# Optimization experiments

Hardware: AMD Instinct MI355X
Metric: run time of the kernel (lower is better)

## Reference

```python
import jax, jax.numpy as jnp
import numpy as np

HIDDEN_DIM = 2048
NUM_EXPERTS = 64
TOP_K = 8
NUM_TOKENS = 16384


def setup_inputs() -> dict:
    key = jax.random.key(0)
    k_x, k_w, k_b = jax.random.split(key, 3)
    X = jax.random.normal(k_x, (NUM_TOKENS, HIDDEN_DIM), dtype=jnp.float32)
    # nn.Linear(hidden_dim, num_experts): weight [out, in], bias [out]
    bound = 1.0 / np.sqrt(HIDDEN_DIM)
    W_gate = jax.random.uniform(k_w, (NUM_EXPERTS, HIDDEN_DIM), jnp.float32, -bound, bound)
    b_gate = jax.random.uniform(k_b, (NUM_EXPERTS,), jnp.float32, -bound, bound)
    return {"X": X, "W_gate": W_gate, "b_gate": b_gate}


def reference(X, W_gate, b_gate):
    # gate linear: [T, H] @ [H, E] + [E] -> [T, E]
    router_logits = jnp.einsum('th,eh->te', X, W_gate) + b_gate
    # softmax in float32 (matches dtype=torch.float)
    router_probs = jax.nn.softmax(router_logits.astype(jnp.float32), axis=-1)
    # top-k over experts: [T, K]
    router_weights, selected_experts_indices = jax.lax.top_k(router_probs, TOP_K)
    router_weights = router_weights / jnp.sum(router_weights, axis=-1, keepdims=True)
    router_weights = router_weights.astype(X.dtype)
    # one-hot [T, K, E] -> permute(2,1,0) -> [E, K, T]
    expert_mask = jax.nn.one_hot(selected_experts_indices, NUM_EXPERTS, dtype=jnp.int64 if jax.config.jax_enable_x64 else jnp.int32)
    expert_mask = jnp.transpose(expert_mask, (2, 1, 0))
    return (router_logits, router_weights, selected_experts_indices.astype(jnp.int32), expert_mask)
```

## Files before the change

### kernel.cpp

```cpp
#include <hip/hip_runtime.h>

#define NT 16384
#define NH 2048
#define NE 64
#define TOPK 8

#define TB 32
#define KSTEPS 64
#define KQ 4
#define KSW (KSTEPS / KQ)

#define LOFF 0
#define WOFF (NT * NE)
#define IOFF (WOFF + NT * TOPK)
#define MOFF (IOFF + NT * TOPK)

typedef __attribute__((ext_vector_type(8))) short short8;
typedef __attribute__((ext_vector_type(4))) float floatx4;

union FragU { uint4 u; short8 s; };

__device__ __forceinline__ unsigned pack3(float a, float b, unsigned& w1, unsigned& w2) {
    unsigned au = __float_as_uint(a), bu = __float_as_uint(b);
    unsigned ah0 = au & 0xFFFF0000u, bh0 = bu & 0xFFFF0000u;
    float ra = a - __uint_as_float(ah0);
    float rb = b - __uint_as_float(bh0);
    unsigned ar = __float_as_uint(ra), br = __float_as_uint(rb);
    unsigned ah1 = ar & 0xFFFF0000u, bh1 = br & 0xFFFF0000u;
    float sa = ra - __uint_as_float(ah1);
    float sb = rb - __uint_as_float(bh1);
    w1 = bh1 | (ah1 >> 16);
    w2 = (__float_as_uint(sb) & 0xFFFF0000u) | (__float_as_uint(sa) >> 16);
    return bh0 | (ah0 >> 16);
}

__global__ __launch_bounds__(64)
void wconv_kernel(const float* __restrict__ Wg, uint4* __restrict__ wsp) {
    const int b = blockIdx.x;
    const int t = b >> 2, g = b & 3;
    const int l = threadIdx.x;
    const int e  = g * 16 + (l & 15);
    const int k0 = t * 32 + (l >> 4) * 8;
    const float* src = Wg + (size_t)e * NH + k0;
    float4 w0 = *(const float4*)src;
    float4 w1 = *(const float4*)(src + 4);
    unsigned u1[4], u2[4];
    uint4 p0;
    p0.x = pack3(w0.x, w0.y, u1[0], u2[0]);
    p0.y = pack3(w0.z, w0.w, u1[1], u2[1]);
    p0.z = pack3(w1.x, w1.y, u1[2], u2[2]);
    p0.w = pack3(w1.z, w1.w, u1[3], u2[3]);
    uint4* dst = wsp + (size_t)((t * 4 + g) * 3) * 64 + l;
    dst[0]   = p0;
    dst[64]  = make_uint4(u1[0], u1[1], u1[2], u1[3]);
    dst[128] = make_uint4(u2[0], u2[1], u2[2], u2[3]);
}

__global__ __launch_bounds__(256, 2)
void router_kernel(const float* __restrict__ X, const uint4* __restrict__ wsp,
                   const float* __restrict__ bg, float* __restrict__ out) {
    __shared__ __align__(16) float P[KQ][TB][68];
    __shared__ __align__(16) float Ls[TB][68];

    const int tid = threadIdx.x;
    const int kh  = tid >> 6;
    const int l   = tid & 63;
    const int lr  = l & 15, lq = l >> 4;
    const int tbase = blockIdx.x * TB;

    floatx4 acc[2][4];
#pragma unroll
    for (int a = 0; a < 2; a++)
#pragma unroll
        for (int g = 0; g < 4; g++) acc[a][g] = (floatx4)0.0f;

    const float* xp0 = X + (size_t)(tbase + lr) * NH + kh * (KSW * 32) + lq * 8;
    const float* xp1 = xp0 + (size_t)16 * NH;
    const uint4* wp = wsp + (size_t)(kh * KSW) * 12 * 64 + l;

    float4 a0lo = *(const float4*)xp0;
    float4 a0hi = *(const float4*)(xp0 + 4);
    float4 a1lo = *(const float4*)xp1;
    float4 a1hi = *(const float4*)(xp1 + 4);

    {
        float4 z = make_float4(0.f, 0.f, 0.f, 0.f);
#pragma unroll
        for (int m = 0; m < 16; m++) {
            int f2  = tid + 256 * m;
            int seg = f2 >> 3;
            int off = (f2 & 7) << 2;
            *(float4*)(out + MOFF + (size_t)seg * NT + tbase + off) = z;
        }
    }

#pragma unroll 2
    for (int t = 0; t < KSW; t++) {
        FragU b[4][3];
        const uint4* wt = wp + t * 768;
#pragma unroll
        for (int g = 0; g < 4; g++)
#pragma unroll
            for (int p = 0; p < 3; p++)
                b[g][p].u = wt[(g * 3 + p) * 64];

        FragU af[2][3];
        {
            unsigned u1[4], u2[4];
            uint4 q;
            q.x = pack3(a0lo.x, a0lo.y, u1[0], u2[0]);
            q.y = pack3(a0lo.z, a0lo.w, u1[1], u2[1]);
            q.z = pack3(a0hi.x, a0hi.y, u1[2], u2[2]);
            q.w = pack3(a0hi.z, a0hi.w, u1[3], u2[3]);
            af[0][0].u = q;
            af[0][1].u = make_uint4(u1[0], u1[1], u1[2], u1[3]);
            af[0][2].u = make_uint4(u2[0], u2[1], u2[2], u2[3]);
            q.x = pack3(a1lo.x, a1lo.y, u1[0], u2[0]);
            q.y = pack3(a1lo.z, a1lo.w, u1[1], u2[1]);
            q.z = pack3(a1hi.x, a1hi.y, u1[2], u2[2]);
            q.w = pack3(a1hi.z, a1hi.w, u1[3], u2[3]);
            af[1][0].u = q;
            af[1][1].u = make_uint4(u1[0], u1[1], u1[2], u1[3]);
            af[1][2].u = make_uint4(u2[0], u2[1], u2[2], u2[3]);
        }

        if (t + 1 < KSW) {
            const float* nx0 = xp0 + (t + 1) * 32;
            const float* nx1 = xp1 + (t + 1) * 32;
            a0lo = *(const float4*)nx0;
            a0hi = *(const float4*)(nx0 + 4);
            a1lo = *(const float4*)nx1;
            a1hi = *(const float4*)(nx1 + 4);
        }

#pragma unroll
        for (int g = 0; g < 4; g++)
#pragma unroll
            for (int a = 0; a < 2; a++) {
                acc[a][g] = __builtin_amdgcn_mfma_f32_16x16x32_bf16(af[a][0].s, b[g][0].s, acc[a][g], 0, 0, 0);
                acc[a][g] = __builtin_amdgcn_mfma_f32_16x16x32_bf16(af[a][0].s, b[g][1].s, acc[a][g], 0, 0, 0);
                acc[a][g] = __builtin_amdgcn_mfma_f32_16x16x32_bf16(af[a][1].s, b[g][0].s, acc[a][g], 0, 0, 0);
                acc[a][g] = __builtin_amdgcn_mfma_f32_16x16x32_bf16(af[a][1].s, b[g][1].s, acc[a][g], 0, 0, 0);
                acc[a][g] = __builtin_amdgcn_mfma_f32_16x16x32_bf16(af[a][0].s, b[g][2].s, acc[a][g], 0, 0, 0);
                acc[a][g] = __builtin_amdgcn_mfma_f32_16x16x32_bf16(af[a][2].s, b[g][0].s, acc[a][g], 0, 0, 0);
            }
    }

#pragma unroll
    for (int a = 0; a < 2; a++)
#pragma unroll
        for (int g = 0; g < 4; g++)
#pragma unroll
            for (int r = 0; r < 4; r++)
                P[kh][a * 16 + lq * 4 + r][g * 16 + lr] = acc[a][g][r];
    __syncthreads();

#pragma unroll
    for (int jj = 0; jj < 2; jj++) {
        int f4  = tid + 256 * jj;
        int tok = f4 >> 4;
        int e4  = (f4 & 15) << 2;
        float4 s0 = *(float4*)&P[0][tok][e4];
        float4 s1 = *(float4*)&P[1][tok][e4];
        float4 s2 = *(float4*)&P[2][tok][e4];
        float4 s3 = *(float4*)&P[3][tok][e4];
        float4 bb = *(const float4*)(bg + e4);
        float4 v;
        v.x = s0.x + s1.x + s2.x + s3.x + bb.x;
        v.y = s0.y + s1.y + s2.y + s3.y + bb.y;
        v.z = s0.z + s1.z + s2.z + s3.z + bb.z;
        v.w = s0.w + s1.w + s2.w + s3.w + bb.w;
        *(float4*)&Ls[tok][e4] = v;
        *(float4*)(out + LOFF + (size_t)tbase * NE + (size_t)f4 * 4) = v;
    }
    __syncthreads();

    const int tok = (tid >> 6) * 8 + ((tid & 63) >> 3);
    const int el  = tid & 7;
    float4 va = *(float4*)&Ls[tok][el * 8];
    float4 vb = *(float4*)&Ls[tok][el * 8 + 4];
    float v[8] = {va.x, va.y, va.z, va.w, vb.x, vb.y, vb.z, vb.w};

    unsigned msk = 0;
    float m0 = 0.f, ssum = 0.f, myv = 0.f;
    int myi = 0;
#pragma unroll
    for (int r = 0; r < 8; r++) {
        float bv = -3.0e38f; int bi = 64;
#pragma unroll
        for (int j = 0; j < 8; j++) {
            bool better = (((msk >> j) & 1u) == 0u) && (v[j] > bv);
            bv = better ? v[j] : bv;
            bi = better ? (el * 8 + j) : bi;
        }
#pragma unroll
        for (int s2 = 1; s2 < 8; s2 <<= 1) {
            float ov = __shfl_xor(bv, s2);
            int   oi = __shfl_xor(bi, s2);
            bool take = (ov > bv) || (ov == bv && oi < bi);
            bv = take ? ov : bv;
            bi = take ? oi : bi;
        }
        if ((bi >> 3) == el) msk |= (1u << (bi & 7));
        if (r == 0) m0 = bv;
        ssum += __expf(bv - m0);
        if (r == el) { myv = bv; myi = bi; }
    }
    float w = __expf(myv - m0) / ssum;
    size_t gt = (size_t)(tbase + tok);
    out[WOFF + gt * TOPK + el] = w;
    out[IOFF + gt * TOPK + el] = (float)myi;
    out[MOFF + (size_t)myi * (TOPK * NT) + (size_t)el * NT + gt] = 1.0f;
}

extern "C" void kernel_launch(void* const* d_in, const int* in_sizes, int n_in,
                              void* d_out, int out_size, void* d_ws, size_t ws_size,
                              hipStream_t stream) {
    const float* X  = (const float*)d_in[0];
    const float* Wg = (const float*)d_in[1];
    const float* bg = (const float*)d_in[2];
    float* out = (float*)d_out;
    uint4* wsp = (uint4*)d_ws;

    hipLaunchKernelGGL(wconv_kernel, dim3(KSTEPS * 4), dim3(64), 0, stream, Wg, wsp);
    hipLaunchKernelGGL(router_kernel, dim3(NT / TB), dim3(256), 0, stream,
                       X, (const uint4*)wsp, bg, out);
}
```

Baseline: 223.2 us.

## Split token halves across doubled wave count and raise MFMA priority

The router kernel now launches 512 threads per block. Each wave handles one 16-token half and one K quarter, where before each wave computed both halves. This halves per-wave accumulator and fragment registers, so occupancy can rise under launch_bounds(512,4). The MFMA block is also wrapped in s_setprio to favor matrix issue. The trade-off is that each wave now loads the W fragments for its own token half, doubling W fragment traffic per block.

After: 241.4 us. 1.08x slower.

```diff
diff --git a/kernel.cpp b/kernel.cpp
--- a/kernel.cpp
+++ b/kernel.cpp
@@ -56,38 +56,35 @@
     dst[128] = make_uint4(u2[0], u2[1], u2[2], u2[3]);
 }
 
-__global__ __launch_bounds__(256, 2)
+__global__ __launch_bounds__(512, 4)
 void router_kernel(const float* __restrict__ X, const uint4* __restrict__ wsp,
                    const float* __restrict__ bg, float* __restrict__ out) {
     __shared__ __align__(16) float P[KQ][TB][68];
     __shared__ __align__(16) float Ls[TB][68];
 
     const int tid = threadIdx.x;
-    const int kh  = tid >> 6;
+    const int w   = tid >> 6;
+    const int kh  = w & 3;
+    const int th  = w >> 2;
     const int l   = tid & 63;
     const int lr  = l & 15, lq = l >> 4;
     const int tbase = blockIdx.x * TB;
 
-    floatx4 acc[2][4];
-#pragma unroll
-    for (int a = 0; a < 2; a++)
-#pragma unroll
-        for (int g = 0; g < 4; g++) acc[a][g] = (floatx4)0.0f;
-
-    const float* xp0 = X + (size_t)(tbase + lr) * NH + kh * (KSW * 32) + lq * 8;
-    const float* xp1 = xp0 + (size_t)16 * NH;
+    floatx4 acc[4];
+#pragma unroll
+    for (int g = 0; g < 4; g++) acc[g] = (floatx4)0.0f;
+
+    const float* xp0 = X + (size_t)(tbase + th * 16 + lr) * NH + kh * (KSW * 32) + lq * 8;
     const uint4* wp = wsp + (size_t)(kh * KSW) * 12 * 64 + l;
 
     float4 a0lo = *(const float4*)xp0;
     float4 a0hi = *(const float4*)(xp0 + 4);
-    float4 a1lo = *(const float4*)xp1;
-    float4 a1hi = *(const float4*)(xp1 + 4);
 
     {
         float4 z = make_float4(0.f, 0.f, 0.f, 0.f);
 #pragma unroll
-        for (int m = 0; m < 16; m++) {
-            int f2  = tid + 256 * m;
+        for (int m = 0; m < 8; m++) {
+            int f2  = tid + 512 * m;
             int seg = f2 >> 3;
             int off = (f2 & 7) << 2;
             *(float4*)(out + MOFF + (size_t)seg * NT + tbase + off) = z;
@@ -104,7 +101,7 @@
             for (int p = 0; p < 3; p++)
                 b[g][p].u = wt[(g * 3 + p) * 64];
 
-        FragU af[2][3];
+        FragU af[3];
         {
             unsigned u1[4], u2[4];
             uint4 q;
@@ -112,52 +109,39 @@
             q.y = pack3(a0lo.z, a0lo.w, u1[1], u2[1]);
             q.z = pack3(a0hi.x, a0hi.y, u1[2], u2[2]);
             q.w = pack3(a0hi.z, a0hi.w, u1[3], u2[3]);
-            af[0][0].u = q;
-            af[0][1].u = make_uint4(u1[0], u1[1], u1[2], u1[3]);
-            af[0][2].u = make_uint4(u2[0], u2[1], u2[2], u2[3]);
-            q.x = pack3(a1lo.x, a1lo.y, u1[0], u2[0]);
-            q.y = pack3(a1lo.z, a1lo.w, u1[1], u2[1]);
-            q.z = pack3(a1hi.x, a1hi.y, u1[2], u2[2]);
-            q.w = pack3(a1hi.z, a1hi.w, u1[3], u2[3]);
-            af[1][0].u = q;
-            af[1][1].u = make_uint4(u1[0], u1[1], u1[2], u1[3]);
-            af[1][2].u = make_uint4(u2[0], u2[1], u2[2], u2[3]);
+            af[0].u = q;
+            af[1].u = make_uint4(u1[0], u1[1], u1[2], u1[3]);
+            af[2].u = make_uint4(u2[0], u2[1], u2[2], u2[3]);
         }
 
         if (t + 1 < KSW) {
             const float* nx0 = xp0 + (t + 1) * 32;
-            const float* nx1 = xp1 + (t + 1) * 32;
             a0lo = *(const float4*)nx0;
             a0hi = *(const float4*)(nx0 + 4);
-            a1lo = *(const float4*)nx1;
-            a1hi = *(const float4*)(nx1 + 4);
-        }
-
-#pragma unroll
-        for (int g = 0; g < 4; g++)
-#pragma unroll
-            for (int a = 0; a < 2; a++) {
-                acc[a][g] = __builtin_amdgcn_mfma_f32_16x16x32_bf16(af[a][0].s, b[g][0].s, acc[a][g], 0, 0, 0);
-                acc[a][g] = __builtin_amdgcn_mfma_f32_16x16x32_bf16(af[a][0].s, b[g][1].s, acc[a][g], 0, 0, 0);
-                acc[a][g] = __builtin_amdgcn_mfma_f32_16x16x32_bf16(af[a][1].s, b[g][0].s, acc[a][g], 0, 0, 0);
-                acc[a][g] = __builtin_amdgcn_mfma_f32_16x16x32_bf16(af[a][1].s, b[g][1].s, acc[a][g], 0, 0, 0);
-                acc[a][g] = __builtin_amdgcn_mfma_f32_16x16x32_bf16(af[a][0].s, b[g][2].s, acc[a][g], 0, 0, 0);
-                acc[a][g] = __builtin_amdgcn_mfma_f32_16x16x32_bf16(af[a][2].s, b[g][0].s, acc[a][g], 0, 0, 0);
-            }
-    }
-
-#pragma unroll
-    for (int a = 0; a < 2; a++)
-#pragma unroll
-        for (int g = 0; g < 4; g++)
-#pragma unroll
-            for (int r = 0; r < 4; r++)
-                P[kh][a * 16 + lq * 4 + r][g * 16 + lr] = acc[a][g][r];
+        }
+
+        __builtin_amdgcn_s_setprio(1);
+#pragma unroll
+        for (int g = 0; g < 4; g++) {
+            acc[g] = __builtin_amdgcn_mfma_f32_16x16x32_bf16(af[0].s, b[g][0].s, acc[g], 0, 0, 0);
+            acc[g] = __builtin_amdgcn_mfma_f32_16x16x32_bf16(af[0].s, b[g][1].s, acc[g], 0, 0, 0);
+            acc[g] = __builtin_amdgcn_mfma_f32_16x16x32_bf16(af[1].s, b[g][0].s, acc[g], 0, 0, 0);
+            acc[g] = __builtin_amdgcn_mfma_f32_16x16x32_bf16(af[1].s, b[g][1].s, acc[g], 0, 0, 0);
+            acc[g] = __builtin_amdgcn_mfma_f32_16x16x32_bf16(af[0].s, b[g][2].s, acc[g], 0, 0, 0);
+            acc[g] = __builtin_amdgcn_mfma_f32_16x16x32_bf16(af[2].s, b[g][0].s, acc[g], 0, 0, 0);
+        }
+        __builtin_amdgcn_s_setprio(0);
+    }
+
+#pragma unroll
+    for (int g = 0; g < 4; g++)
+#pragma unroll
+        for (int r = 0; r < 4; r++)
+            P[kh][th * 16 + lq * 4 + r][g * 16 + lr] = acc[g][r];
     __syncthreads();
 
-#pragma unroll
-    for (int jj = 0; jj < 2; jj++) {
-        int f4  = tid + 256 * jj;
+    {
+        int f4  = tid;
         int tok = f4 >> 4;
         int e4  = (f4 & 15) << 2;
         float4 s0 = *(float4*)&P[0][tok][e4];
@@ -175,42 +159,44 @@
     }
     __syncthreads();
 
-    const int tok = (tid >> 6) * 8 + ((tid & 63) >> 3);
-    const int el  = tid & 7;
-    float4 va = *(float4*)&Ls[tok][el * 8];
-    float4 vb = *(float4*)&Ls[tok][el * 8 + 4];
-    float v[8] = {va.x, va.y, va.z, va.w, vb.x, vb.y, vb.z, vb.w};
-
-    unsigned msk = 0;
-    float m0 = 0.f, ssum = 0.f, myv = 0.f;
-    int myi = 0;
-#pragma unroll
-    for (int r = 0; r < 8; r++) {
-        float bv = -3.0e38f; int bi = 64;
-#pragma unroll
-        for (int j = 0; j < 8; j++) {
-            bool better = (((msk >> j) & 1u) == 0u) && (v[j] > bv);
-            bv = better ? v[j] : bv;
-            bi = better ? (el * 8 + j) : bi;
-        }
-#pragma unroll
-        for (int s2 = 1; s2 < 8; s2 <<= 1) {
-            float ov = __shfl_xor(bv, s2);
-            int   oi = __shfl_xor(bi, s2);
-            bool take = (ov > bv) || (ov == bv && oi < bi);
-            bv = take ? ov : bv;
-            bi = take ? oi : bi;
-        }
-        if ((bi >> 3) == el) msk |= (1u << (bi & 7));
-        if (r == 0) m0 = bv;
-        ssum += __expf(bv - m0);
-        if (r == el) { myv = bv; myi = bi; }
-    }
-    float w = __expf(myv - m0) / ssum;
-    size_t gt = (size_t)(tbase + tok);
-    out[WOFF + gt * TOPK + el] = w;
-    out[IOFF + gt * TOPK + el] = (float)myi;
-    out[MOFF + (size_t)myi * (TOPK * NT) + (size_t)el * NT + gt] = 1.0f;
+    if (tid < 256) {
+        const int tok = tid >> 3;
+        const int el  = tid & 7;
+        float4 va = *(float4*)&Ls[tok][el * 8];
+        float4 vb = *(float4*)&Ls[tok][el * 8 + 4];
+        float v[8] = {va.x, va.y, va.z, va.w, vb.x, vb.y, vb.z, vb.w};
+
+        unsigned msk = 0;
+        float m0 = 0.f, ssum = 0.f, myv = 0.f;
+        int myi = 0;
+#pragma unroll
+        for (int r = 0; r < 8; r++) {
+            float bv = -3.0e38f; int bi = 64;
+#pragma unroll
+            for (int j = 0; j < 8; j++) {
+                bool better = (((msk >> j) & 1u) == 0u) && (v[j] > bv);
+                bv = better ? v[j] : bv;
+                bi = better ? (el * 8 + j) : bi;
+            }
+#pragma unroll
+            for (int s2 = 1; s2 < 8; s2 <<= 1) {
+                float ov = __shfl_xor(bv, s2);
+                int   oi = __shfl_xor(bi, s2);
+                bool take = (ov > bv) || (ov == bv && oi < bi);
+                bv = take ? ov : bv;
+                bi = take ? oi : bi;
+            }
+            if ((bi >> 3) == el) msk |= (1u << (bi & 7));
+            if (r == 0) m0 = bv;
+            ssum += __expf(bv - m0);
+            if (r == el) { myv = bv; myi = bi; }
+        }
+        float wgt = __expf(myv - m0) / ssum;
+        size_t gt = (size_t)(tbase + tok);
+        out[WOFF + gt * TOPK + el] = wgt;
+        out[IOFF + gt * TOPK + el] = (float)myi;
+        out[MOFF + (size_t)myi * (TOPK * NT) + (size_t)el * NT + gt] = 1.0f;
+    }
 }
 
 extern "C" void kernel_launch(void* const* d_in, const int* in_sizes, int n_in,
@@ -223,6 +209,6 @@
     uint4* wsp = (uint4*)d_ws;
 
     hipLaunchKernelGGL(wconv_kernel, dim3(KSTEPS * 4), dim3(64), 0, stream, Wg, wsp);
-    hipLaunchKernelGGL(router_kernel, dim3(NT / TB), dim3(256), 0, stream,
+    hipLaunchKernelGGL(router_kernel, dim3(NT / TB), dim3(512), 0, stream,
                        X, (const uint4*)wsp, bg, out);
 }
```
